# Optimization experiments

Hardware: AMD Instinct MI355X
Metric: run time of the kernel (lower is better)

## Reference

```python
import jax, jax.numpy as jnp
import numpy as np

DEPTH = 2
EPS = 1e-12

def _l2norm(x, axis=-1):
    n = jnp.sqrt(jnp.sum(x * x, axis=axis, keepdims=True))
    return x / jnp.maximum(n, EPS)

def setup_inputs() -> dict:
    key = jax.random.key(0)
    k1, k2, k3, k4, k5 = jax.random.split(key, 5)
    N, D, R, E = 50000, 100, 1000, 800000
    features = jax.random.normal(k1, (N, D), dtype=jnp.float32)
    rel_emb = jax.random.normal(k2, (R, D), dtype=jnp.float32)
    none_relation = jax.random.normal(k3, (D,), dtype=jnp.float32)
    # edge list sorted by destination row (matches coalesced sparse layout
    # assumed by the original: softmax values align with edge order)
    rows = jnp.sort(jax.random.randint(k4, (E,), 0, N))
    cols = jax.random.randint(k5, (E,), 0, N)
    adj_index = jnp.stack([rows, cols], axis=1).astype(jnp.int64)
    return {"features": features, "rel_emb": rel_emb,
            "adj_index": adj_index, "none_relation": none_relation}

def reference(features, rel_emb, adj_index, none_relation):
    N = features.shape[0]
    rows = adj_index[:, 0]  # destination (softmax segment, scatter target)
    cols = adj_index[:, 1]  # neighbor (gather source)
    feats = jnp.tanh(features)
    outputs = [feats]
    nr = _l2norm(none_relation, axis=0)  # [D]
    for _ in range(DEPTH):
        neighs = feats[cols]                      # [E, D] gather
        score = -jnp.einsum('ed,d->e', _l2norm(neighs), nr)  # [E]
        # sparse softmax over each destination row's edges
        m = jax.ops.segment_max(score, rows, num_segments=N)
        e = jnp.exp(score - m[rows])
        denom = jax.ops.segment_sum(e, rows, num_segments=N)
        att = e / denom[rows]                     # [E]
        new_feats = jax.ops.segment_sum(neighs * att[:, None], rows,
                                        num_segments=N)  # [N, D]
        feats = jnp.tanh(new_feats)
        outputs.append(feats)
    return jnp.concatenate(outputs, axis=1)  # [N, D*(DEPTH+1)]
```

## Files before the change

kernel.cpp:

```cpp
#include <hip/hip_runtime.h>
#include <hip/hip_fp16.h>
#include <math.h>

#define D_FEAT 100
#define ROW_STRIDE 300
#define ROWB 112u

__device__ __forceinline__ float fast_tanh(float x) {
    float ax = fabsf(x);
    float e  = __expf(2.f * ax);
    float t  = 1.f - 2.f / (e + 1.f);
    return copysignf(t, x);
}

__device__ __forceinline__ unsigned pb4(float x0, float x1, float x2, float x3) {
    unsigned b0 = (unsigned)(int)rintf(fmaf(x0, 127.f, 128.f));
    unsigned b1 = (unsigned)(int)rintf(fmaf(x1, 127.f, 128.f));
    unsigned b2 = (unsigned)(int)rintf(fmaf(x2, 127.f, 128.f));
    unsigned b3 = (unsigned)(int)rintf(fmaf(x3, 127.f, 128.f));
    return b0 | (b1 << 8) | (b2 << 16) | (b3 << 24);
}

__device__ __forceinline__ float half_reduce(float v) {
    #pragma unroll
    for (int off = 16; off; off >>= 1) v += __shfl_xor(v, off, 64);
    return v;
}

__global__ __launch_bounds__(256) void tanh_score_kernel(
    const float* __restrict__ features,
    float* __restrict__ out,
    unsigned char* __restrict__ tab0,
    float* __restrict__ escore0,
    const float* __restrict__ none_rel,
    const int* __restrict__ adj,
    int* __restrict__ startArr,
    int* __restrict__ cols,
    int E, int N)
{
    int gtid = blockIdx.x * blockDim.x + threadIdx.x;
    if (gtid < E && cols) cols[gtid] = adj[2 * gtid + 1];
    if (gtid <= N) {
        if (gtid == N) startArr[N] = E;
        else {
            int lo = 0, hi = E;
            while (lo < hi) {
                int mid = (lo + hi) >> 1;
                if (adj[2 * mid] < gtid) lo = mid + 1; else hi = mid;
            }
            startArr[gtid] = lo;
        }
    }

    int waveId = gtid >> 6;
    int lane = threadIdx.x & 63;
    int h32  = lane >> 5;
    int l    = lane & 31;
    int n    = waveId * 2 + h32;
    const bool valid_n = (n < N);
    const bool fact = valid_n && (l >= 1) && (l <= 25);

    float x0 = 0.f, x1 = 0.f, x2 = 0.f, x3 = 0.f;
    if (fact) {
        float4 f = ((const float4*)(features + (size_t)n * D_FEAT))[l - 1];
        x0 = fast_tanh(f.x); x1 = fast_tanh(f.y);
        x2 = fast_tanh(f.z); x3 = fast_tanh(f.w);
        ((float4*)(out + (size_t)n * ROW_STRIDE))[l - 1] = make_float4(x0, x1, x2, x3);
    }
    if (tab0 && valid_n) {
        unsigned char* row = tab0 + (size_t)n * ROWB;
        if (l >= 1 && l <= 25) {
            *(unsigned*)(row + 4 * (l - 1)) = pb4(x0, x1, x2, x3);
        } else if (l == 26) {
            *(unsigned*)(row + 100) = 0x80808080u;
            *(unsigned long long*)(row + 104) = 0x8080808080808080ull;
        }
    }

    float nx = 0.f, ny = 0.f, nz = 0.f, nw = 0.f;
    if (l >= 1 && l <= 25) {
        float4 v = ((const float4*)none_rel)[l - 1];
        nx = v.x; ny = v.y; nz = v.z; nw = v.w;
    }
    float ss = half_reduce(nx * nx + ny * ny + nz * nz + nw * nw);
    float inv_nr = 1.f / fmaxf(sqrtf(ss), 1e-12f);

    float dot = half_reduce(x0 * nx + x1 * ny + x2 * nz + x3 * nw) * inv_nr;
    float sq  = half_reduce(x0 * x0 + x1 * x1 + x2 * x2 + x3 * x3);
    if (l == 0 && valid_n) {
        float es = __expf(-dot / fmaxf(sqrtf(sq), 1e-12f));
        escore0[n] = es;
    }
}

template <bool WRITE_TAB>
__global__ __launch_bounds__(256) void attn8_kernel(
    const unsigned char* __restrict__ tab,
    float* __restrict__ outp,
    unsigned char* __restrict__ tab_out,
    const int* __restrict__ cols,
    const int* __restrict__ start,
    const float* __restrict__ esc_in,
    float* __restrict__ esc_out,
    const float* __restrict__ none_rel,
    int N)
{
    const int waveId = (int)((blockIdx.x * blockDim.x + threadIdx.x) >> 6);
    const int lane = threadIdx.x & 63;
    const int h32  = lane >> 5;
    const int hl   = lane & 31;
    const int base = h32 << 5;
    const int n    = waveId * 2 + h32;
    const bool valid_n = (n < N);

    const int grp = hl / 7;
    const int li  = hl - 7 * grp;
    const unsigned suboff = (unsigned)(li * 16);

    int e0 = 0, e1 = 0;
    if (valid_n) { e0 = start[n]; e1 = start[n + 1]; }
    const int deg = e1 - e0;
    int maxdeg = deg;
    { int o = __shfl_xor(maxdeg, 32, 64); maxdeg = maxdeg > o ? maxdeg : o; }

    int   c0 = 0, c1 = 0;
    float w0 = 0.f, w1 = 0.f;
    if (hl < deg)      { c0 = cols[e0 + hl];      w0 = esc_in[c0]; }
    if (hl + 32 < deg) { c1 = cols[e0 + hl + 32]; w1 = esc_in[c1]; }

    float dsum = half_reduce(w0 + w1);

    float a[16];
    #pragma unroll
    for (int k = 0; k < 16; ++k) a[k] = 0.f;

#define ACC16(V, W)                                                           \
    {                                                                         \
        unsigned _d;                                                          \
        _d = (V).x;                                                           \
        a[0]  = fmaf((float)(_d & 255u),         (W), a[0]);                  \
        a[1]  = fmaf((float)((_d >> 8) & 255u),  (W), a[1]);                  \
        a[2]  = fmaf((float)((_d >> 16) & 255u), (W), a[2]);                  \
        a[3]  = fmaf((float)(_d >> 24),          (W), a[3]);                  \
        _d = (V).y;                                                           \
        a[4]  = fmaf((float)(_d & 255u),         (W), a[4]);                  \
        a[5]  = fmaf((float)((_d >> 8) & 255u),  (W), a[5]);                  \
        a[6]  = fmaf((float)((_d >> 16) & 255u), (W), a[6]);                  \
        a[7]  = fmaf((float)(_d >> 24),          (W), a[7]);                  \
        _d = (V).z;                                                           \
        a[8]  = fmaf((float)(_d & 255u),         (W), a[8]);                  \
        a[9]  = fmaf((float)((_d >> 8) & 255u),  (W), a[9]);                  \
        a[10] = fmaf((float)((_d >> 16) & 255u), (W), a[10]);                 \
        a[11] = fmaf((float)(_d >> 24),          (W), a[11]);                 \
        _d = (V).w;                                                           \
        a[12] = fmaf((float)(_d & 255u),         (W), a[12]);                 \
        a[13] = fmaf((float)((_d >> 8) & 255u),  (W), a[13]);                 \
        a[14] = fmaf((float)((_d >> 16) & 255u), (W), a[14]);                 \
        a[15] = fmaf((float)(_d >> 24),          (W), a[15]);                 \
    }

#define BATCH8(CST, WST, SRCB)                                                \
    {                                                                         \
        const int sA = base + (SRCB) + grp;                                   \
        const int sB = base + (SRCB) + 4 + grp;                               \
        int   cA = __shfl((CST), sA, 64), cB = __shfl((CST), sB, 64);         \
        float wA = __shfl((WST), sA, 64), wB = __shfl((WST), sB, 64);         \
        const uint4 vA = *(const uint4*)(tab + (size_t)((unsigned)cA * ROWB + suboff)); \
        const uint4 vB = *(const uint4*)(tab + (size_t)((unsigned)cB * ROWB + suboff)); \
        ACC16(vA, wA) ACC16(vB, wB)                                           \
    }

    const int cap1 = maxdeg < 32 ? maxdeg : 32;
    for (int r = 0; r < cap1; r += 8) BATCH8(c0, w0, r)
    const int cap2 = maxdeg < 64 ? maxdeg : 64;
    for (int r = 32; r < cap2; r += 8) BATCH8(c1, w1, r - 32)
#undef BATCH8

    for (int e = e0 + 64; e < e1; ++e) {
        int   c = cols[e];
        float w = esc_in[c];
        const uint4 v = *(const uint4*)(tab + (size_t)((unsigned)c * ROWB + suboff));
        if (grp == 0) ACC16(v, w)
        dsum += w;
    }
#undef ACC16

    const int p1 = base + hl + ((hl < 14) ? 14 : 0);
    #pragma unroll
    for (int k = 0; k < 16; ++k) a[k] += __shfl(a[k], p1, 64);
    const int p2 = base + hl + ((hl < 7) ? 7 : 0);
    #pragma unroll
    for (int k = 0; k < 16; ++k) a[k] += __shfl(a[k], p2, 64);

    const float invd = (deg > 0) ? 1.f / (127.f * dsum) : 0.f;
    const float bsh  = (deg > 0) ? (-128.f / 127.f) : 0.f;
    float r[16];
    #pragma unroll
    for (int k = 0; k < 16; ++k) {
        r[k] = fast_tanh(fmaf(a[k], invd, bsh));
        if (!(valid_n) || (16 * hl + k) >= 100) r[k] = 0.f;
    }

    if (valid_n && hl < 7) {
        float4* orow = (float4*)(outp + (size_t)n * ROW_STRIDE);
        #pragma unroll
        for (int j = 0; j < 4; ++j) {
            if (j == 0 || hl < 6)
                orow[4 * hl + j] = make_float4(r[4*j], r[4*j+1], r[4*j+2], r[4*j+3]);
        }
        if constexpr (WRITE_TAB) {
            unsigned char* trow = tab_out + (size_t)n * ROWB;
            *(uint4*)(trow + 16 * hl) = make_uint4(
                pb4(r[0],  r[1],  r[2],  r[3]),
                pb4(r[4],  r[5],  r[6],  r[7]),
                pb4(r[8],  r[9],  r[10], r[11]),
                pb4(r[12], r[13], r[14], r[15]));
        }
    }

    if constexpr (WRITE_TAB) {
        float nn[16];
        #pragma unroll
        for (int k = 0; k < 16; ++k) nn[k] = 0.f;
        if (hl < 7) {
            #pragma unroll
            for (int j = 0; j < 4; ++j) {
                if (j == 0 || hl < 6) {
                    float4 u = *(const float4*)(none_rel + 16 * hl + 4 * j);
                    nn[4*j] = u.x; nn[4*j+1] = u.y; nn[4*j+2] = u.z; nn[4*j+3] = u.w;
                }
            }
        }
        float ssl = 0.f, dotl = 0.f, sql = 0.f;
        #pragma unroll
        for (int k = 0; k < 16; ++k) {
            ssl  += nn[k] * nn[k];
            dotl += r[k] * nn[k];
            sql  += r[k] * r[k];
        }
        float ss  = half_reduce(ssl);
        float inv_nr = 1.f / fmaxf(sqrtf(ss), 1e-12f);
        float dot = half_reduce(dotl) * inv_nr;
        float sq  = half_reduce(sql);
        if (hl == 0 && valid_n) {
            float es = __expf(-dot / fmaxf(sqrtf(sq), 1e-12f));
            esc_out[n] = es;
        }
    }
}

__global__ __launch_bounds__(256) void attn_f32_kernel(
    const float* __restrict__ prev,
    float* __restrict__ outp,
    const int2* __restrict__ adj2,
    const int* __restrict__ start,
    const float* __restrict__ escore_in,
    float* __restrict__ escore_out,
    const float* __restrict__ none_rel,
    int N)
{
    int waveId = (int)((blockIdx.x * blockDim.x + threadIdx.x) >> 6);
    int lane = threadIdx.x & 63;
    int h32  = lane >> 5;
    int l    = lane & 31;
    int n    = waveId * 2 + h32;
    const bool valid_n = (n < N);
    const bool fact = valid_n && (l >= 1) && (l <= 25);
    const int base = h32 << 5;

    int e0 = 0, e1 = 0;
    if (valid_n) { e0 = start[n]; e1 = start[n + 1]; }
    const int deg = e1 - e0;

    int   c0 = 0, c1 = 0;
    float w0 = 0.f, w1 = 0.f;
    if (l < deg)      { c0 = adj2[e0 + l].y;      w0 = escore_in[c0]; }
    if (l + 32 < deg) { c1 = adj2[e0 + l + 32].y; w1 = escore_in[c1]; }

    int maxdeg = deg;
    { int o = __shfl_xor(maxdeg, 32, 64); maxdeg = maxdeg > o ? maxdeg : o; }

    float d_acc = 0.f, a0 = 0.f, a1 = 0.f, a2 = 0.f, a3 = 0.f;
    const int cap1 = maxdeg < 32 ? maxdeg : 32;
    for (int r = 0; r < cap1; r += 8) {
        #pragma unroll
        for (int j = 0; j < 8; ++j) {
            int   i = r + j;
            int   c = __shfl(c0, base + i, 64);
            float w = __shfl(w0, base + i, 64);
            float p0 = 0.f, p1 = 0.f, p2 = 0.f, p3 = 0.f;
            if (fact && (i < deg)) {
                float4 v = ((const float4*)(prev + (size_t)c * ROW_STRIDE))[l - 1];
                p0 = v.x; p1 = v.y; p2 = v.z; p3 = v.w;
            }
            if (i >= deg) w = 0.f;
            d_acc += w;
            a0 += w * p0; a1 += w * p1; a2 += w * p2; a3 += w * p3;
        }
    }
    const int cap2 = maxdeg < 64 ? maxdeg : 64;
    for (int r = 32; r < cap2; r += 8) {
        #pragma unroll
        for (int j = 0; j < 8; ++j) {
            int   i = r + j;
            int   c = __shfl(c1, base + i - 32, 64);
            float w = __shfl(w1, base + i - 32, 64);
            float p0 = 0.f, p1 = 0.f, p2 = 0.f, p3 = 0.f;
            if (fact && (i < deg)) {
                float4 v = ((const float4*)(prev + (size_t)c * ROW_STRIDE))[l - 1];
                p0 = v.x; p1 = v.y; p2 = v.z; p3 = v.w;
            }
            if (i >= deg) w = 0.f;
            d_acc += w;
            a0 += w * p0; a1 += w * p1; a2 += w * p2; a3 += w * p3;
        }
    }
    for (int e = e0 + 64; e < e1; ++e) {
        int c = adj2[e].y;
        float w = escore_in[c];
        float p0 = 0.f, p1 = 0.f, p2 = 0.f, p3 = 0.f;
        if (fact) {
            float4 v = ((const float4*)(prev + (size_t)c * ROW_STRIDE))[l - 1];
            p0 = v.x; p1 = v.y; p2 = v.z; p3 = v.w;
        }
        d_acc += w;
        a0 += w * p0; a1 += w * p1; a2 += w * p2; a3 += w * p3;
    }

    const float inv_d = (deg > 0) ? 1.f / d_acc : 0.f;
    float r0 = fast_tanh(a0 * inv_d);
    float r1 = fast_tanh(a1 * inv_d);
    float r2 = fast_tanh(a2 * inv_d);
    float r3 = fast_tanh(a3 * inv_d);
    if (fact) {
        ((float4*)(outp + (size_t)n * ROW_STRIDE))[l - 1] = make_float4(r0, r1, r2, r3);
    } else {
        r0 = r1 = r2 = r3 = 0.f;
    }

    if (escore_out) {
        float nx = 0.f, ny = 0.f, nz = 0.f, nw = 0.f;
        if (l >= 1 && l <= 25) {
            float4 v = ((const float4*)none_rel)[l - 1];
            nx = v.x; ny = v.y; nz = v.z; nw = v.w;
        }
        float ss = half_reduce(nx * nx + ny * ny + nz * nz + nw * nw);
        float inv_nr = 1.f / fmaxf(sqrtf(ss), 1e-12f);
        float dot = half_reduce(r0 * nx + r1 * ny + r2 * nz + r3 * nw) * inv_nr;
        float sq  = half_reduce(r0 * r0 + r1 * r1 + r2 * r2 + r3 * r3);
        if (l == 0 && valid_n) {
            float es = __expf(-dot / fmaxf(sqrtf(sq), 1e-12f));
            escore_out[n] = es;
        }
    }
}

extern "C" void kernel_launch(void* const* d_in, const int* in_sizes, int n_in,
                              void* d_out, int out_size, void* d_ws, size_t ws_size,
                              hipStream_t stream) {
    const float* features = (const float*)d_in[0];
    const int*   adj      = (const int*)d_in[2];
    const float* none_rel = (const float*)d_in[3];
    float* out = (float*)d_out;

    const int N = in_sizes[0] / D_FEAT;
    const int E = in_sizes[2] / 2;

    size_t off = 0;
    auto take = [&](size_t bytes) { size_t o = off; off = (off + bytes + 15) & ~(size_t)15; return o; };
    char* w = (char*)d_ws;
    int*   start   = (int*)  (w + take(sizeof(int)   * (size_t)(N + 1)));
    float* escore0 = (float*)(w + take(sizeof(float) * (size_t)N));
    float* escore1 = (float*)(w + take(sizeof(float) * (size_t)N));
    int*   cols    = (int*)  (w + take(sizeof(int)   * (size_t)E));
    size_t tab_off0 = take((size_t)N * ROWB);
    size_t tab_off1 = take((size_t)N * ROWB);
    const bool use_tab = (ws_size >= off);
    unsigned char* tab0 = use_tab ? (unsigned char*)(w + tab_off0) : nullptr;
    unsigned char* tab1 = use_tab ? (unsigned char*)(w + tab_off1) : nullptr;

    const int pairs = (N + 1) / 2;
    const int node_blocks = (pairs * 64 + 255) / 256;
    const int2* adj2 = (const int2*)adj;

    tanh_score_kernel<<<node_blocks, 256, 0, stream>>>(features, out, tab0,
                                                       escore0, none_rel,
                                                       adj, start,
                                                       use_tab ? cols : nullptr,
                                                       E, N);
    if (use_tab) {
        attn8_kernel<true><<<node_blocks, 256, 0, stream>>>(
            tab0, out + D_FEAT, tab1, cols, start, escore0, escore1, none_rel, N);
        attn8_kernel<false><<<node_blocks, 256, 0, stream>>>(
            tab1, out + 2 * D_FEAT, nullptr, cols, start, escore1, nullptr, none_rel, N);
    } else {
        attn_f32_kernel<<<node_blocks, 256, 0, stream>>>(
            out, out + D_FEAT, adj2, start, escore0, escore1, none_rel, N);
        attn_f32_kernel<<<node_blocks, 256, 0, stream>>>(
            out + D_FEAT, out + 2 * D_FEAT, adj2, start, escore1, nullptr, none_rel, N);
    }
}
```

Baseline: 161.5 us.

## Pad quantized feature table rows to 128 bytes and gather 4 edges per batch

Feature table rows in the 8-bit quantized layout are padded from 112 to 128 bytes, so each gathered row fills one aligned 128-byte line. Eight lanes now cover a row and four groups each take one edge, instead of seven lanes and 4.57 groups. Offsets become shifts, the lane reduction becomes xor shuffles, and each batch now issues four row loads instead of two. In exchange the table uses more memory bandwidth, and a new alignment check can make the code fall back to the slow path when the workspace base is not 128-byte aligned.

```diff
diff --git a/kernel.cpp b/kernel.cpp
--- a/kernel.cpp
+++ b/kernel.cpp
@@ -4,7 +4,7 @@
 
 #define D_FEAT 100
 #define ROW_STRIDE 300
-#define ROWB 112u
+#define ROWB 128u
 
 __device__ __forceinline__ float fast_tanh(float x) {
     float ax = fabsf(x);
@@ -68,12 +68,13 @@
         ((float4*)(out + (size_t)n * ROW_STRIDE))[l - 1] = make_float4(x0, x1, x2, x3);
     }
     if (tab0 && valid_n) {
-        unsigned char* row = tab0 + (size_t)n * ROWB;
+        unsigned char* row = tab0 + ((size_t)n << 7);
         if (l >= 1 && l <= 25) {
             *(unsigned*)(row + 4 * (l - 1)) = pb4(x0, x1, x2, x3);
-        } else if (l == 26) {
-            *(unsigned*)(row + 100) = 0x80808080u;
-            *(unsigned long long*)(row + 104) = 0x8080808080808080ull;
+        } else if (l >= 26) {
+            *(unsigned*)(row + 4 * (l - 1)) = 0x80808080u;
+        } else {
+            *(unsigned*)(row + 124) = 0x80808080u;
         }
     }
 
@@ -113,9 +114,8 @@
     const int n    = waveId * 2 + h32;
     const bool valid_n = (n < N);
 
-    const int grp = hl / 7;
-    const int li  = hl - 7 * grp;
-    const unsigned suboff = (unsigned)(li * 16);
+    const int grp = hl >> 3;
+    const unsigned suboff = (unsigned)((hl & 7) << 4);
 
     int e0 = 0, e1 = 0;
     if (valid_n) { e0 = start[n]; e1 = start[n + 1]; }
@@ -159,38 +159,39 @@
         a[15] = fmaf((float)(_d >> 24),          (W), a[15]);                 \
     }
 
-#define BATCH8(CST, WST, SRCB)                                                \
+#define BATCH16(CST, WST, RBASE)                                              \
     {                                                                         \
-        const int sA = base + (SRCB) + grp;                                   \
-        const int sB = base + (SRCB) + 4 + grp;                               \
-        int   cA = __shfl((CST), sA, 64), cB = __shfl((CST), sB, 64);         \
-        float wA = __shfl((WST), sA, 64), wB = __shfl((WST), sB, 64);         \
-        const uint4 vA = *(const uint4*)(tab + (size_t)((unsigned)cA * ROWB + suboff)); \
-        const uint4 vB = *(const uint4*)(tab + (size_t)((unsigned)cB * ROWB + suboff)); \
-        ACC16(vA, wA) ACC16(vB, wB)                                           \
+        const int s0 = base + (RBASE) + grp;                                  \
+        int   cA = __shfl((CST), s0,      64), cB = __shfl((CST), s0 + 4, 64);\
+        int   cC = __shfl((CST), s0 + 8,  64), cD = __shfl((CST), s0 + 12,64);\
+        float wA = __shfl((WST), s0,      64), wB = __shfl((WST), s0 + 4, 64);\
+        float wC = __shfl((WST), s0 + 8,  64), wD = __shfl((WST), s0 + 12,64);\
+        const uint4 vA = *(const uint4*)(tab + (((size_t)(unsigned)cA) << 7) + suboff); \
+        const uint4 vB = *(const uint4*)(tab + (((size_t)(unsigned)cB) << 7) + suboff); \
+        const uint4 vC = *(const uint4*)(tab + (((size_t)(unsigned)cC) << 7) + suboff); \
+        const uint4 vD = *(const uint4*)(tab + (((size_t)(unsigned)cD) << 7) + suboff); \
+        ACC16(vA, wA) ACC16(vB, wB) ACC16(vC, wC) ACC16(vD, wD)               \
     }
 
     const int cap1 = maxdeg < 32 ? maxdeg : 32;
-    for (int r = 0; r < cap1; r += 8) BATCH8(c0, w0, r)
+    for (int r = 0; r < cap1; r += 16) BATCH16(c0, w0, r)
     const int cap2 = maxdeg < 64 ? maxdeg : 64;
-    for (int r = 32; r < cap2; r += 8) BATCH8(c1, w1, r - 32)
-#undef BATCH8
+    for (int r = 32; r < cap2; r += 16) BATCH16(c1, w1, r - 32)
+#undef BATCH16
 
     for (int e = e0 + 64; e < e1; ++e) {
         int   c = cols[e];
         float w = esc_in[c];
-        const uint4 v = *(const uint4*)(tab + (size_t)((unsigned)c * ROWB + suboff));
+        const uint4 v = *(const uint4*)(tab + (((size_t)(unsigned)c) << 7) + suboff);
         if (grp == 0) ACC16(v, w)
         dsum += w;
     }
 #undef ACC16
 
-    const int p1 = base + hl + ((hl < 14) ? 14 : 0);
     #pragma unroll
-    for (int k = 0; k < 16; ++k) a[k] += __shfl(a[k], p1, 64);
-    const int p2 = base + hl + ((hl < 7) ? 7 : 0);
+    for (int k = 0; k < 16; ++k) a[k] += __shfl_xor(a[k], 16, 64);
     #pragma unroll
-    for (int k = 0; k < 16; ++k) a[k] += __shfl(a[k], p2, 64);
+    for (int k = 0; k < 16; ++k) a[k] += __shfl_xor(a[k], 8, 64);
 
     const float invd = (deg > 0) ? 1.f / (127.f * dsum) : 0.f;
     const float bsh  = (deg > 0) ? (-128.f / 127.f) : 0.f;
@@ -198,18 +199,20 @@
     #pragma unroll
     for (int k = 0; k < 16; ++k) {
         r[k] = fast_tanh(fmaf(a[k], invd, bsh));
-        if (!(valid_n) || (16 * hl + k) >= 100) r[k] = 0.f;
-    }
-
-    if (valid_n && hl < 7) {
-        float4* orow = (float4*)(outp + (size_t)n * ROW_STRIDE);
-        #pragma unroll
-        for (int j = 0; j < 4; ++j) {
-            if (j == 0 || hl < 6)
-                orow[4 * hl + j] = make_float4(r[4*j], r[4*j+1], r[4*j+2], r[4*j+3]);
+        if (!valid_n || hl >= 8 || (16 * hl + k) >= 100) r[k] = 0.f;
+    }
+
+    if (valid_n && hl < 8) {
+        if (hl < 7) {
+            float4* orow = (float4*)(outp + (size_t)n * ROW_STRIDE);
+            #pragma unroll
+            for (int j = 0; j < 4; ++j) {
+                if (j == 0 || hl < 6)
+                    orow[4 * hl + j] = make_float4(r[4*j], r[4*j+1], r[4*j+2], r[4*j+3]);
+            }
         }
         if constexpr (WRITE_TAB) {
-            unsigned char* trow = tab_out + (size_t)n * ROWB;
+            unsigned char* trow = tab_out + ((size_t)n << 7);
             *(uint4*)(trow + 16 * hl) = make_uint4(
                 pb4(r[0],  r[1],  r[2],  r[3]),
                 pb4(r[4],  r[5],  r[6],  r[7]),
@@ -367,7 +370,7 @@
     const int E = in_sizes[2] / 2;
 
     size_t off = 0;
-    auto take = [&](size_t bytes) { size_t o = off; off = (off + bytes + 15) & ~(size_t)15; return o; };
+    auto take = [&](size_t bytes) { size_t o = off; off = (off + bytes + 127) & ~(size_t)127; return o; };
     char* w = (char*)d_ws;
     int*   start   = (int*)  (w + take(sizeof(int)   * (size_t)(N + 1)));
     float* escore0 = (float*)(w + take(sizeof(float) * (size_t)N));
@@ -375,7 +378,8 @@
     int*   cols    = (int*)  (w + take(sizeof(int)   * (size_t)E));
     size_t tab_off0 = take((size_t)N * ROWB);
     size_t tab_off1 = take((size_t)N * ROWB);
-    const bool use_tab = (ws_size >= off);
+    const bool use_tab = (ws_size >= off) &&
+                         ((((uintptr_t)w) & 127) == 0);
     unsigned char* tab0 = use_tab ? (unsigned char*)(w + tab_off0) : nullptr;
     unsigned char* tab1 = use_tab ? (unsigned char*)(w + tab_off1) : nullptr;
 
```

Result: slower. 168.2 us (+4.2%).
